# Optimization experiments

Hardware: AMD Instinct MI355X
Metric: run time of the kernel (lower is better)

Reference implementation:

```python
import jax, jax.numpy as jnp
import numpy as np
import math


def _silu(v):
    return v * jax.nn.sigmoid(v)


def setup_inputs() -> dict:
    key = jax.random.key(0)
    ks = jax.random.split(key, 8)
    b, l = 4, 2048
    dim, hidden, d_state, dt_rank = 1024, 2048, 16, 64
    s = 0.02
    x = jax.random.normal(ks[0], (b, l, dim), dtype=jnp.float32)
    W_in = jax.random.normal(ks[1], (2 * hidden, dim), dtype=jnp.float32) * s
    conv_w = jax.random.normal(ks[2], (hidden, 1, 3), dtype=jnp.float32) * s  # depthwise, k=3
    conv_b = jnp.zeros((hidden,), dtype=jnp.float32)
    W_xproj = jax.random.normal(ks[3], (dt_rank + 2 * d_state, hidden), dtype=jnp.float32) * s
    W_dt = jax.random.uniform(ks[4], (hidden, dt_rank), minval=-1.0 / dt_rank, maxval=1.0 / dt_rank, dtype=jnp.float32)
    dt_init = jnp.exp(jax.random.uniform(ks[5], (hidden,), dtype=jnp.float32) * (math.log(0.1) - math.log(0.001)) + math.log(0.001))
    b_dt = -1.0 / dt_init  # matches dt_proj.bias init in source
    A_log = -jnp.arange(1, d_state + 1, dtype=jnp.float32)
    D = jnp.ones((hidden,), dtype=jnp.float32)
    W_out = jax.random.normal(ks[6], (dim, hidden), dtype=jnp.float32) * s
    return {"x": x, "W_in": W_in, "conv_w": conv_w, "conv_b": conv_b,
            "W_xproj": W_xproj, "W_dt": W_dt, "b_dt": b_dt,
            "A_log": A_log, "D": D, "W_out": W_out}


def reference(x, W_in, conv_w, conv_b, W_xproj, W_dt, b_dt, A_log, D, W_out):
    b, l, dim = x.shape
    hidden = W_dt.shape[0]
    dt_rank = W_dt.shape[1]
    d_state = A_log.shape[0]

    # in_proj and chunk into (x, z)
    xz = jnp.einsum('bld,ed->ble', x, W_in)  # (b, l, 2*hidden)
    u, z = jnp.split(xz, 2, axis=-1)

    # depthwise conv1d, kernel 3, symmetric padding 1 (non-causal, as in source)
    uc = jax.lax.conv_general_dilated(
        jnp.moveaxis(u, 1, 2), conv_w, window_strides=(1,), padding=[(1, 1)],
        dimension_numbers=('NCH', 'OIH', 'NCH'), feature_group_count=hidden)
    uc = jnp.moveaxis(uc + conv_b[None, :, None], 1, 2)  # (b, l, hidden)
    uc = _silu(uc)

    # x_proj -> (dt, B, C)
    x_dbl = jnp.einsum('blh,eh->ble', uc, W_xproj)
    dtp = x_dbl[..., :dt_rank]
    Bm = x_dbl[..., dt_rank:dt_rank + d_state]   # (b, l, n)
    Cm = x_dbl[..., dt_rank + d_state:]          # (b, l, n)
    dt = jax.nn.softplus(jnp.einsum('blr,hr->blh', dtp, W_dt) + b_dt)  # (b, l, hidden)

    A = -jnp.exp(A_log)  # (n,)

    # selective scan: h_{k} = exp(dt_k * A) * h_{k-1} + B_k (outer) u_k ; y_k = C_k . h_k
    def step(h, inp):
        u_t, dt_t, B_t, C_t = inp  # (b,h), (b,h), (b,n), (b,n)
        dA = jnp.exp(dt_t[:, None, :] * A[None, :, None])      # (b, n, h)
        h = dA * h + B_t[:, :, None] * u_t[:, None, :]         # (b, n, h)
        y_t = jnp.einsum('bn,bnh->bh', C_t, h)
        return h, y_t

    xs = (jnp.moveaxis(uc, 0, 1), jnp.moveaxis(dt, 0, 1),
          jnp.moveaxis(Bm, 0, 1), jnp.moveaxis(Cm, 0, 1))
    h0 = jnp.zeros((b, d_state, hidden), dtype=uc.dtype)
    _, ys = jax.lax.scan(step, h0, xs)
    y = jnp.moveaxis(ys, 0, 1) + D * uc  # skip term D*u

    y = y * _silu(z)
    out = jnp.einsum('blh,dh->bld', y, W_out)
    return x + out
```

## Files before the change

### kernel.cpp

```cpp
#include <hip/hip_runtime.h>
#include <cmath>

typedef unsigned short u16;
typedef __bf16 bf16x8 __attribute__((ext_vector_type(8)));
typedef float f32x4 __attribute__((ext_vector_type(4)));
typedef unsigned short u16x8 __attribute__((ext_vector_type(8)));

#define NB_B   4
#define NB_L   2048
#define NB_DIM 1024
#define NB_H   2048
#define NB_NS  16
#define NB_DTR 64
#define NB_TOK (NB_B * NB_L)
#define NCHUNK 64
#define CLEN   32

__device__ __forceinline__ u16 f2b(float f) {
  union { float f; unsigned u; } v; v.f = f;
  unsigned r = v.u + 0x7fffu + ((v.u >> 16) & 1u);
  return (u16)(r >> 16);
}
__device__ __forceinline__ float b2f(u16 h) {
  union { unsigned u; float f; } v; v.u = ((unsigned)h) << 16;
  return v.f;
}
__device__ __forceinline__ float exp_small(float w) {
  return __builtin_fmaf(w, __builtin_fmaf(w, 0.5f, 1.0f), 1.0f);
}

#define CVT_N0 2097152
#define CVT_N1 (CVT_N0 + 1048576)
#define CVT_N2 (CVT_N1 + 32768)
#define CVT_N3 (CVT_N2 + 524288)
__global__ void cvt_all_k(const float* __restrict__ x, const float* __restrict__ W_in,
                          const float* __restrict__ W_dt, const float* __restrict__ W_out,
                          u16* __restrict__ xb, u16* __restrict__ winb,
                          u16* __restrict__ wdtb, u16* __restrict__ woutb) {
  int i = blockIdx.x * 256 + threadIdx.x;
  const float* src; u16* dst; int off;
  if (i < CVT_N0)      { src = x;     dst = xb;    off = i; }
  else if (i < CVT_N1) { src = W_in;  dst = winb;  off = i - CVT_N0; }
  else if (i < CVT_N2) { src = W_dt;  dst = wdtb;  off = i - CVT_N1; }
  else                 { src = W_out; dst = woutb; off = i - CVT_N2; }
  float4 v = reinterpret_cast<const float4*>(src)[off];
  ushort4 o;
  o.x = f2b(v.x); o.y = f2b(v.y); o.z = f2b(v.z); o.w = f2b(v.w);
  reinterpret_cast<ushort4*>(dst)[off] = o;
}

__global__ void cvt_pad_xproj_k(const float* __restrict__ in, u16* __restrict__ out) {
  int i = blockIdx.x * 256 + threadIdx.x;
  int r = i >> 11, c = i & 2047;
  out[i] = (r < 96) ? f2b(in[r * 2048 + c]) : (u16)0;
}

__global__ void extract_dtp_k(const float* __restrict__ xdbl, u16* __restrict__ out) {
  int i = blockIdx.x * 256 + threadIdx.x;
  int r = i >> 6, c = i & 63;
  out[i] = f2b(xdbl[r * 128 + c]);
}

#define EPI_BF16    0
#define EPI_F32     1
#define EPI_SP_BF16 2
#define EPI_RES_F32 3

__device__ __forceinline__ void stage16(const u16* g, u16* l) {
  __builtin_amdgcn_global_load_lds(
      (const __attribute__((address_space(1))) unsigned int*)g,
      (__attribute__((address_space(3))) unsigned int*)l, 16, 0, 0);
}

template <int EPI, int BM>
__global__ __launch_bounds__(512, 1)
void gemm8p_k(const u16* __restrict__ A, const u16* __restrict__ Bm,
              int K, int ldc,
              u16* __restrict__ outB, float* __restrict__ outF,
              const float* __restrict__ bias, const float* __restrict__ resid,
              int gx) {
  constexpr int BN = 256;
  constexpr int MR = BM / 32;
  constexpr int MH = MR / 2;
  constexpr int HA = BM / 2;
  constexpr int LA = BM / 128;
  constexpr int L  = 2 * LA + 4;
  constexpr int BUFE = (BM + BN) * 64;
  __shared__ u16 smem[2 * BUFE];

  const int tid  = threadIdx.x;
  const int lane = tid & 63;
  const int wave = tid >> 6;
  const int wr = wave >> 2, wc = wave & 3;
  const int fr = lane & 15, fq = lane >> 4;

  const int nwg = gridDim.x;
  const int cpx = nwg >> 3;
  const int bid = blockIdx.x;
  const int id2 = (bid & 7) * cpx + (bid >> 3);
  const int row0 = (id2 % gx) * BM;
  const int col0 = (id2 / gx) * BN;

  f32x4 acc[MR][4] = {};
  bf16x8 bB[4][2], bA0[MH][2], bA1[MH][2];

  auto STAGE_B = [&](int kt) {
    const int k0 = kt * 64;
    u16* base = smem + (kt & 1) * BUFE + BM * 64;
#pragma unroll
    for (int h = 0; h < 2; ++h)
#pragma unroll
      for (int l = 0; l < 2; ++l) {
        int c = l * 512 + tid;
        int rih = c >> 3, p = c & 7;
        stage16(Bm + (size_t)(col0 + h * 128 + rih) * K + k0 + ((p ^ (rih & 7)) * 8),
                base + (h * 128 + rih) * 64 + p * 8);
      }
  };
  auto STAGE_A = [&](int kt) {
    const int k0 = kt * 64;
    u16* base = smem + (kt & 1) * BUFE;
#pragma unroll
    for (int h = 0; h < 2; ++h)
#pragma unroll
      for (int l = 0; l < LA; ++l) {
        int c = l * 512 + tid;
        int rih = c >> 3, p = c & 7;
        stage16(A + (size_t)(row0 + h * HA + rih) * K + k0 + ((p ^ (rih & 7)) * 8),
                base + (h * HA + rih) * 64 + p * 8);
      }
  };
  auto LD_A = [&](int m, int kk, int bi) {
    int rt = wr * HA + m * 16 + fr;
    int p = (kk * 4 + fq) ^ (rt & 7);
    return *reinterpret_cast<const bf16x8*>(smem + bi * BUFE + rt * 64 + p * 8);
  };
  auto LD_B = [&](int n, int kk, int bi) {
    int rt = wc * 64 + n * 16 + fr;
    int p = (kk * 4 + fq) ^ (rt & 7);
    return *reinterpret_cast<const bf16x8*>(smem + bi * BUFE + BM * 64 + rt * 64 + p * 8);
  };

  const int nk = K >> 6;
  STAGE_B(0); STAGE_A(0);
  if (nk > 1) { STAGE_B(1); STAGE_A(1); }
  if (nk > 1) asm volatile("s_waitcnt vmcnt(%0)" :: "i"(L) : "memory");
  else        asm volatile("s_waitcnt vmcnt(0)" ::: "memory");
  __builtin_amdgcn_s_barrier();
  __builtin_amdgcn_sched_barrier(0);
#pragma unroll
  for (int n = 0; n < 4; ++n) { bB[n][0] = LD_B(n, 0, 0); bB[n][1] = LD_B(n, 1, 0); }
#pragma unroll
  for (int m = 0; m < MH; ++m) { bA0[m][0] = LD_A(m, 0, 0); bA0[m][1] = LD_A(m, 1, 0); }
  asm volatile("s_waitcnt lgkmcnt(0)" ::: "memory");
  __builtin_amdgcn_s_barrier();
  __builtin_amdgcn_sched_barrier(0);

  for (int kt = 0; kt < nk; ++kt) {
    const int bi = kt & 1;
    if (kt + 2 < nk) STAGE_B(kt + 2);
    __builtin_amdgcn_s_setprio(1);
#pragma unroll
    for (int m = 0; m < MH; ++m)
#pragma unroll
      for (int n = 0; n < 2; ++n)
#pragma unroll
        for (int kk = 0; kk < 2; ++kk)
          acc[m][n] = __builtin_amdgcn_mfma_f32_16x16x32_bf16(bA0[m][kk], bB[n][kk], acc[m][n], 0, 0, 0);
    __builtin_amdgcn_s_setprio(0);
    __builtin_amdgcn_sched_barrier(0);
#pragma unroll
    for (int m = 0; m < MH; ++m) { bA1[m][0] = LD_A(MH + m, 0, bi); bA1[m][1] = LD_A(MH + m, 1, bi); }
    __builtin_amdgcn_s_setprio(1);
#pragma unroll
    for (int m = 0; m < MH; ++m)
#pragma unroll
      for (int n = 2; n < 4; ++n)
#pragma unroll
        for (int kk = 0; kk < 2; ++kk)
          acc[m][n] = __builtin_amdgcn_mfma_f32_16x16x32_bf16(bA0[m][kk], bB[n][kk], acc[m][n], 0, 0, 0);
    __builtin_amdgcn_s_setprio(0);
    asm volatile("s_waitcnt lgkmcnt(0)" ::: "memory");
    __builtin_amdgcn_s_barrier();
    __builtin_amdgcn_sched_barrier(0);
    if (kt + 2 < nk) STAGE_A(kt + 2);
    __builtin_amdgcn_s_setprio(1);
#pragma unroll
    for (int m = 0; m < MH; ++m)
#pragma unroll
      for (int n = 0; n < 2; ++n)
#pragma unroll
        for (int kk = 0; kk < 2; ++kk)
          acc[MH + m][n] = __builtin_amdgcn_mfma_f32_16x16x32_bf16(bA1[m][kk], bB[n][kk], acc[MH + m][n], 0, 0, 0);
    __builtin_amdgcn_s_setprio(0);
    __builtin_amdgcn_sched_barrier(0);
    if (kt + 1 < nk) {
      if (kt + 2 < nk) asm volatile("s_waitcnt vmcnt(%0)" :: "i"(L) : "memory");
      else             asm volatile("s_waitcnt vmcnt(0)" ::: "memory");
      __builtin_amdgcn_s_barrier();
      __builtin_amdgcn_sched_barrier(0);
#pragma unroll
      for (int n = 0; n < 2; ++n) { bB[n][0] = LD_B(n, 0, bi ^ 1); bB[n][1] = LD_B(n, 1, bi ^ 1); }
#pragma unroll
      for (int m = 0; m < MH; ++m) { bA0[m][0] = LD_A(m, 0, bi ^ 1); bA0[m][1] = LD_A(m, 1, bi ^ 1); }
    }
    __builtin_amdgcn_s_setprio(1);
#pragma unroll
    for (int m = 0; m < MH; ++m)
#pragma unroll
      for (int n = 2; n < 4; ++n)
#pragma unroll
        for (int kk = 0; kk < 2; ++kk)
          acc[MH + m][n] = __builtin_amdgcn_mfma_f32_16x16x32_bf16(bA1[m][kk], bB[n][kk], acc[MH + m][n], 0, 0, 0);
    __builtin_amdgcn_s_setprio(0);
    if (kt + 1 < nk) {
#pragma unroll
      for (int n = 2; n < 4; ++n) { bB[n][0] = LD_B(n, 0, bi ^ 1); bB[n][1] = LD_B(n, 1, bi ^ 1); }
    }
    asm volatile("s_waitcnt lgkmcnt(0)" ::: "memory");
    __builtin_amdgcn_s_barrier();
    __builtin_amdgcn_sched_barrier(0);
  }

  if constexpr (EPI == EPI_BF16 || EPI == EPI_SP_BF16) {
    float* wv = reinterpret_cast<float*>(smem) + wave * 1024;
#pragma unroll
    for (int m = 0; m < MR; ++m) {
#pragma unroll
      for (int n = 0; n < 4; ++n) {
        const int c = col0 + wc * 64 + n * 16 + fr;
        float bv = (EPI == EPI_SP_BF16) ? bias[c] : 0.f;
#pragma unroll
        for (int j = 0; j < 4; ++j) {
          float v = acc[m][n][j];
          if (EPI == EPI_SP_BF16) {
            float xx = v + bv;
            float t = __expf(xx);
            float sp = (xx > -5.f) ? log1pf(t) : t;
            v = (xx > 20.f) ? xx : sp;
          }
          wv[(fq * 4 + j) * 64 + n * 16 + fr] = v;
        }
      }
#pragma unroll
      for (int p = 0; p < 2; ++p) {
        const int rf = p * 8 + (lane >> 3);
        const int c0 = (lane & 7) * 8;
        const float* rp = wv + rf * 64 + c0;
        u16x8 o;
#pragma unroll
        for (int k = 0; k < 8; ++k) o[k] = f2b(rp[k]);
        const int grow = row0 + wr * HA + m * 16 + rf;
        const int gcol = col0 + wc * 64 + c0;
        *reinterpret_cast<u16x8*>(&outB[(size_t)grow * ldc + gcol]) = o;
      }
    }
  } else {
#pragma unroll
    for (int m = 0; m < MR; ++m) {
      const int r = row0 + wr * HA + m * 16 + fq * 4;
#pragma unroll
      for (int n = 0; n < 4; ++n) {
        const int c = col0 + wc * 64 + n * 16 + fr;
#pragma unroll
        for (int j = 0; j < 4; ++j) {
          size_t o = (size_t)(r + j) * ldc + c;
          if (EPI == EPI_F32) outF[o] = acc[m][n][j];
          else                outF[o] = acc[m][n][j] + resid[o];
        }
      }
    }
  }
}

template <int EPI, int BM, int BN>
__global__ __launch_bounds__(256)
void gemm_bt_k(const u16* __restrict__ A, const u16* __restrict__ Bm,
               int K, int ldc,
               u16* __restrict__ outB, float* __restrict__ outF,
               const float* __restrict__ bias, const float* __restrict__ resid) {
  constexpr int MR = BM / 32, NR = BN / 32;
  __shared__ u16 smem[(BM + BN) * 32];
  u16* As = smem;
  u16* Bs = smem + BM * 32;
  const int tid  = threadIdx.x;
  const int lane = tid & 63;
  const int wave = tid >> 6;
  const int wr = wave >> 1, wc = wave & 1;
  const int row0 = blockIdx.x * BM;
  const int col0 = blockIdx.y * BN;
  f32x4 acc[MR][NR] = {};

  const int r_ld = tid >> 2;
  const int kb   = (((tid & 3) ^ ((tid >> 3) & 3)) * 8);
  const size_t a_base = (size_t)(row0 + r_ld) * K + kb;
  const size_t b_base = (size_t)(col0 + r_ld) * K + kb;
  u16* lA = As + tid * 8;
  u16* lB = Bs + tid * 8;

  const int fr = lane & 15;
  const int fq = lane >> 4;
  const int fkx = ((fq ^ ((fr >> 1) & 3)) * 8);

  const int nk = K >> 5;
  for (int kt = 0; kt < nk; ++kt) {
    const int k0 = kt * 32;
    __syncthreads();
#pragma unroll
    for (int hh = 0; hh < BM / 64; ++hh)
      stage16(A + a_base + (size_t)(hh * 64) * K + k0, lA + hh * 64 * 32);
#pragma unroll
    for (int hh = 0; hh < BN / 64; ++hh)
      stage16(Bm + b_base + (size_t)(hh * 64) * K + k0, lB + hh * 64 * 32);
    __syncthreads();
    bf16x8 af[MR], bfr[NR];
#pragma unroll
    for (int m = 0; m < MR; ++m)
      af[m] = *reinterpret_cast<const bf16x8*>(&As[(wr * (BM / 2) + m * 16 + fr) * 32 + fkx]);
#pragma unroll
    for (int n = 0; n < NR; ++n)
      bfr[n] = *reinterpret_cast<const bf16x8*>(&Bs[(wc * (BN / 2) + n * 16 + fr) * 32 + fkx]);
#pragma unroll
    for (int m = 0; m < MR; ++m)
#pragma unroll
      for (int n = 0; n < NR; ++n)
        acc[m][n] = __builtin_amdgcn_mfma_f32_16x16x32_bf16(af[m], bfr[n], acc[m][n], 0, 0, 0);
  }

#pragma unroll
  for (int m = 0; m < MR; ++m) {
    const int r = row0 + wr * (BM / 2) + m * 16 + fq * 4;
#pragma unroll
    for (int n = 0; n < NR; ++n) {
      const int c = col0 + wc * (BN / 2) + n * 16 + fr;
#pragma unroll
      for (int j = 0; j < 4; ++j) {
        float v = acc[m][n][j];
        size_t o = (size_t)(r + j) * ldc + c;
        if (EPI == EPI_F32) outF[o] = v;
        else if (EPI == EPI_RES_F32) outF[o] = v + resid[o];
      }
    }
  }
}

__global__ void dwconv_silu_k(const u16* __restrict__ xz, const float* __restrict__ cw,
                              const float* __restrict__ cb, u16* __restrict__ uc) {
  int i = blockIdx.x * 256 + threadIdx.x;
  int hb = i & (NB_H / 8 - 1);
  int t = i >> 8;
  int l = t & (NB_L - 1);
  int h0 = hb * 8;
  const u16* base = xz + (size_t)t * 4096 + h0;
  u16x8 vm = *reinterpret_cast<const u16x8*>(base);
  u16x8 vq = {}, vp = {};
  if (l > 0)          vq = *reinterpret_cast<const u16x8*>(base - 4096);
  if (l < NB_L - 1)   vp = *reinterpret_cast<const u16x8*>(base + 4096);
  u16x8 o;
#pragma unroll
  for (int j = 0; j < 8; ++j) {
    int h = h0 + j;
    float acc = cb[h];
    acc = __builtin_fmaf(b2f(vq[j]), cw[h * 3 + 0], acc);
    acc = __builtin_fmaf(b2f(vm[j]), cw[h * 3 + 1], acc);
    acc = __builtin_fmaf(b2f(vp[j]), cw[h * 3 + 2], acc);
    float s = acc / (1.f + __expf(-acc));
    o[j] = f2b(s);
  }
  *reinterpret_cast<u16x8*>(uc + (size_t)t * NB_H + h0) = o;
}

__global__ __launch_bounds__(256)
void scan_passA_k(const u16* __restrict__ dt, const u16* __restrict__ uc,
                  const float* __restrict__ xdbl, const float* __restrict__ A_log,
                  float* __restrict__ Pout, float* __restrict__ Sout) {
  __shared__ float bc[CLEN][32];
  const int tid = threadIdx.x;
  int idx = blockIdx.x * 256 + tid;
  int h = idx & (NB_H - 1);
  int ck = (idx >> 11) & (NCHUNK - 1);
  int b = idx >> 17;
  const int t0 = b * NB_L + ck * CLEN;
  {
    int r = tid >> 3, q = tid & 7;
    *reinterpret_cast<float4*>(&bc[r][q * 4]) =
        *reinterpret_cast<const float4*>(xdbl + (size_t)(t0 + r) * 128 + 64 + q * 4);
  }
  float An[NB_NS];
#pragma unroll
  for (int n = 0; n < NB_NS; ++n) An[n] = -__expf(A_log[n]);
  float P[NB_NS], S[NB_NS];
#pragma unroll
  for (int n = 0; n < NB_NS; ++n) { P[n] = 1.f; S[n] = 0.f; }
  __syncthreads();
  const u16* up = uc + (size_t)t0 * NB_H + h;
  const u16* dp = dt + (size_t)t0 * NB_H + h;
  float uA = b2f(up[0]),       dA = b2f(dp[0]);
  float uB = b2f(up[NB_H]),    dB = b2f(dp[NB_H]);
  for (int tt = 0; tt < CLEN; ++tt) {
    float uC = 0.f, dC = 0.f;
    if (tt + 2 < CLEN) { uC = b2f(up[2 * NB_H]); dC = b2f(dp[2 * NB_H]); }
    up += NB_H; dp += NB_H;
    float4 B0 = *reinterpret_cast<const float4*>(&bc[tt][0]);
    float4 B1 = *reinterpret_cast<const float4*>(&bc[tt][4]);
    float4 B2 = *reinterpret_cast<const float4*>(&bc[tt][8]);
    float4 B3 = *reinterpret_cast<const float4*>(&bc[tt][12]);
    const float Bf[NB_NS] = {B0.x, B0.y, B0.z, B0.w, B1.x, B1.y, B1.z, B1.w,
                             B2.x, B2.y, B2.z, B2.w, B3.x, B3.y, B3.z, B3.w};
#pragma unroll
    for (int n = 0; n < NB_NS; ++n) {
      float e = exp_small(dA * An[n]);
      P[n] *= e;
      S[n] = __builtin_fmaf(e, S[n], Bf[n] * uA);
    }
    uA = uB; dA = dB; uB = uC; dB = dC;
  }
#pragma unroll
  for (int n = 0; n < NB_NS; ++n) {
    size_t o = ((((size_t)b * NCHUNK + ck) * NB_NS + n) * NB_H + h);
    Pout[o] = P[n]; Sout[o] = S[n];
  }
}

__global__ void scan_passB_k(float* __restrict__ P, const float* __restrict__ S) {
  int idx = blockIdx.x * 256 + threadIdx.x;
  int h = idx & (NB_H - 1);
  int n = (idx >> 11) & (NB_NS - 1);
  int b = idx >> 15;
  const size_t stride = (size_t)NB_NS * NB_H;
  size_t o = ((size_t)b * NCHUNK * NB_NS + n) * NB_H + h;
  float hs = 0.f;
  float p0 = P[o], s0 = S[o];
  for (int ck = 0; ck < NCHUNK; ++ck) {
    float p1 = 0.f, s1 = 0.f;
    if (ck + 1 < NCHUNK) { p1 = P[o + stride]; s1 = S[o + stride]; }
    P[o] = hs;
    hs = __builtin_fmaf(p0, hs, s0);
    o += stride; p0 = p1; s0 = s1;
  }
}

__global__ __launch_bounds__(256)
void scan_passC_k(const u16* __restrict__ dt, const u16* __restrict__ uc,
                  const float* __restrict__ xdbl, const u16* __restrict__ xz,
                  const float* __restrict__ A_log, const float* __restrict__ Dp,
                  const float* __restrict__ Hst, u16* __restrict__ ybf) {
  __shared__ float bc[CLEN][32];
  const int tid = threadIdx.x;
  int idx = blockIdx.x * 256 + tid;
  int h = idx & (NB_H - 1);
  int ck = (idx >> 11) & (NCHUNK - 1);
  int b = idx >> 17;
  const int t0 = b * NB_L + ck * CLEN;
  {
    int r = tid >> 3, q = tid & 7;
    *reinterpret_cast<float4*>(&bc[r][q * 4]) =
        *reinterpret_cast<const float4*>(xdbl + (size_t)(t0 + r) * 128 + 64 + q * 4);
  }
  float An[NB_NS];
#pragma unroll
  for (int n = 0; n < NB_NS; ++n) An[n] = -__expf(A_log[n]);
  float s[NB_NS];
#pragma unroll
  for (int n = 0; n < NB_NS; ++n)
    s[n] = Hst[((((size_t)b * NCHUNK + ck) * NB_NS + n) * NB_H + h)];
  const float Dh = Dp[h];
  __syncthreads();
  const u16* up = uc + (size_t)t0 * NB_H + h;
  const u16* dp = dt + (size_t)t0 * NB_H + h;
  const u16* zp = xz + (size_t)t0 * 4096 + NB_H + h;
  u16* yp = ybf + (size_t)t0 * NB_H + h;
  float uA = b2f(up[0]),    dA = b2f(dp[0]),    zA = b2f(zp[0]);
  float uB = b2f(up[NB_H]), dB = b2f(dp[NB_H]), zB = b2f(zp[4096]);
  for (int tt = 0; tt < CLEN; ++tt) {
    float uC = 0.f, dC = 0.f, zC = 0.f;
    if (tt + 2 < CLEN) {
      uC = b2f(up[2 * NB_H]); dC = b2f(dp[2 * NB_H]); zC = b2f(zp[2 * 4096]);
    }
    up += NB_H; dp += NB_H; zp += 4096;
    float4 B0 = *reinterpret_cast<const float4*>(&bc[tt][0]);
    float4 B1 = *reinterpret_cast<const float4*>(&bc[tt][4]);
    float4 B2 = *reinterpret_cast<const float4*>(&bc[tt][8]);
    float4 B3 = *reinterpret_cast<const float4*>(&bc[tt][12]);
    float4 C0 = *reinterpret_cast<const float4*>(&bc[tt][16]);
    float4 C1 = *reinterpret_cast<const float4*>(&bc[tt][20]);
    float4 C2 = *reinterpret_cast<const float4*>(&bc[tt][24]);
    float4 C3 = *reinterpret_cast<const float4*>(&bc[tt][28]);
    const float Bf[NB_NS] = {B0.x, B0.y, B0.z, B0.w, B1.x, B1.y, B1.z, B1.w,
                             B2.x, B2.y, B2.z, B2.w, B3.x, B3.y, B3.z, B3.w};
    const float Cf[NB_NS] = {C0.x, C0.y, C0.z, C0.w, C1.x, C1.y, C1.z, C1.w,
                             C2.x, C2.y, C2.z, C2.w, C3.x, C3.y, C3.z, C3.w};
    float y = 0.f;
#pragma unroll
    for (int n = 0; n < NB_NS; ++n) {
      float e = exp_small(dA * An[n]);
      s[n] = __builtin_fmaf(e, s[n], Bf[n] * uA);
      y = __builtin_fmaf(Cf[n], s[n], y);
    }
    float v = __builtin_fmaf(Dh, uA, y);
    float g = zA / (1.f + __expf(-zA));
    *yp = f2b(v * g);
    yp += NB_H;
    uA = uB; dA = dB; zA = zB; uB = uC; dB = dC; zB = zC;
  }
}

extern "C" void kernel_launch(void* const* d_in, const int* in_sizes, int n_in,
                              void* d_out, int out_size, void* d_ws, size_t ws_size,
                              hipStream_t stream) {
  const float* x      = (const float*)d_in[0];
  const float* W_in   = (const float*)d_in[1];
  const float* conv_w = (const float*)d_in[2];
  const float* conv_b = (const float*)d_in[3];
  const float* W_xprj = (const float*)d_in[4];
  const float* W_dt   = (const float*)d_in[5];
  const float* b_dt   = (const float*)d_in[6];
  const float* A_log  = (const float*)d_in[7];
  const float* Dp     = (const float*)d_in[8];
  const float* W_out  = (const float*)d_in[9];
  float* out = (float*)d_out;

  char* ws = (char*)d_ws;
  size_t off = 0;
  auto alloc = [&](size_t bytes) {
    void* p = ws + off;
    off += (bytes + 255) & ~(size_t)255;
    return p;
  };
  u16*   xz_b   = (u16*)alloc((size_t)NB_TOK * 4096 * 2);
  u16*   x_b    = (u16*)alloc((size_t)NB_TOK * NB_DIM * 2);
  u16*   win_b  = (u16*)alloc((size_t)4096 * NB_DIM * 2);
  u16*   wxp_b  = (u16*)alloc((size_t)128 * NB_H * 2);
  u16*   wdt_b  = (u16*)alloc((size_t)NB_H * NB_DTR * 2);
  u16*   wout_b = (u16*)alloc((size_t)NB_DIM * NB_H * 2);
  u16*   uc_b   = (u16*)alloc((size_t)NB_TOK * NB_H * 2);
  float* xdbl   = (float*)alloc((size_t)NB_TOK * 128 * 4);
  u16*   dtp_b  = (u16*)alloc((size_t)NB_TOK * NB_DTR * 2);
  u16*   dt_b   = (u16*)alloc((size_t)NB_TOK * NB_H * 2);
  float* scP    = (float*)alloc((size_t)NB_B * NCHUNK * NB_NS * NB_H * 4);
  float* scS    = (float*)alloc((size_t)NB_B * NCHUNK * NB_NS * NB_H * 4);
  u16*   y_b    = (u16*)scS;
  (void)ws_size; (void)in_sizes; (void)n_in; (void)out_size;

  cvt_all_k<<<CVT_N3 / 256, 256, 0, stream>>>(x, W_in, W_dt, W_out, x_b, win_b, wdt_b, wout_b);
  cvt_pad_xproj_k<<<1024, 256, 0, stream>>>(W_xprj, wxp_b);

  gemm8p_k<EPI_BF16, 256><<<512, 512, 0, stream>>>(
      x_b, win_b, NB_DIM, 4096, xz_b, nullptr, nullptr, nullptr, 32);

  dwconv_silu_k<<<(NB_TOK * NB_H / 8) / 256, 256, 0, stream>>>(xz_b, conv_w, conv_b, uc_b);

  gemm_bt_k<EPI_F32, 64, 64><<<dim3(128, 2), 256, 0, stream>>>(
      uc_b, wxp_b, NB_H, 128, nullptr, xdbl, nullptr, nullptr);

  extract_dtp_k<<<(NB_TOK * NB_DTR) / 256, 256, 0, stream>>>(xdbl, dtp_b);

  gemm8p_k<EPI_SP_BF16, 256><<<256, 512, 0, stream>>>(
      dtp_b, wdt_b, NB_DTR, NB_H, dt_b, nullptr, b_dt, nullptr, 32);

  scan_passA_k<<<(NB_B * NCHUNK * NB_H) / 256, 256, 0, stream>>>(dt_b, uc_b, xdbl, A_log, scP, scS);
  scan_passB_k<<<(NB_B * NB_NS * NB_H) / 256, 256, 0, stream>>>(scP, scS);
  scan_passC_k<<<(NB_B * NCHUNK * NB_H) / 256, 256, 0, stream>>>(dt_b, uc_b, xdbl, xz_b, A_log, Dp, scP, y_b);

  gemm8p_k<EPI_RES_F32, 128><<<256, 512, 0, stream>>>(
      y_b, wout_b, NB_H, NB_DIM, nullptr, out, nullptr, x, 64);
}
```

Before: 349.0 us.

## Store scan chunk states in bf16, remap GEMM tiles per XCD, pack epilogue as bf16

The chunk-state buffers exchanged between the three scan passes are stored as bf16 instead of fp32, with the decay product kept as 1-P to preserve precision near one. This halves the traffic between the passes. Each GEMM workgroup now maps to a tile region chosen per XCD (cr/cc/ncx parameters) so tiles on the same die share A and B panels in L2. The bf16 epilogue also converts before staging through padded LDS, which halves LDS traffic. The scan-state rounding to bf16 risks accuracy loss over 64 chunks.

```diff
diff --git a/kernel.cpp b/kernel.cpp
--- a/kernel.cpp
+++ b/kernel.cpp
@@ -78,14 +78,13 @@
               int K, int ldc,
               u16* __restrict__ outB, float* __restrict__ outF,
               const float* __restrict__ bias, const float* __restrict__ resid,
-              int gx) {
-  constexpr int BN = 256;
+              int cr, int cc, int ncx) {
   constexpr int MR = BM / 32;
   constexpr int MH = MR / 2;
   constexpr int HA = BM / 2;
   constexpr int LA = BM / 128;
   constexpr int L  = 2 * LA + 4;
-  constexpr int BUFE = (BM + BN) * 64;
+  constexpr int BUFE = (BM + 256) * 64;
   __shared__ u16 smem[2 * BUFE];
 
   const int tid  = threadIdx.x;
@@ -94,12 +93,10 @@
   const int wr = wave >> 2, wc = wave & 3;
   const int fr = lane & 15, fq = lane >> 4;
 
-  const int nwg = gridDim.x;
-  const int cpx = nwg >> 3;
   const int bid = blockIdx.x;
-  const int id2 = (bid & 7) * cpx + (bid >> 3);
-  const int row0 = (id2 % gx) * BM;
-  const int col0 = (id2 / gx) * BN;
+  const int e = bid & 7, w = bid >> 3;
+  const int row0 = ((e / ncx) * cr + (w % cr)) * BM;
+  const int col0 = ((e % ncx) * cc + (w / cr)) * 256;
 
   f32x4 acc[MR][4] = {};
   bf16x8 bB[4][2], bA0[MH][2], bA1[MH][2];
@@ -223,7 +220,7 @@
   }
 
   if constexpr (EPI == EPI_BF16 || EPI == EPI_SP_BF16) {
-    float* wv = reinterpret_cast<float*>(smem) + wave * 1024;
+    u16* wv = smem + wave * 1152;
 #pragma unroll
     for (int m = 0; m < MR; ++m) {
 #pragma unroll
@@ -239,20 +236,17 @@
             float sp = (xx > -5.f) ? log1pf(t) : t;
             v = (xx > 20.f) ? xx : sp;
           }
-          wv[(fq * 4 + j) * 64 + n * 16 + fr] = v;
+          wv[(fq * 4 + j) * 72 + n * 16 + fr] = f2b(v);
         }
       }
 #pragma unroll
       for (int p = 0; p < 2; ++p) {
         const int rf = p * 8 + (lane >> 3);
         const int c0 = (lane & 7) * 8;
-        const float* rp = wv + rf * 64 + c0;
-        u16x8 o;
-#pragma unroll
-        for (int k = 0; k < 8; ++k) o[k] = f2b(rp[k]);
+        u16x8 ov = *reinterpret_cast<const u16x8*>(wv + rf * 72 + c0);
         const int grow = row0 + wr * HA + m * 16 + rf;
         const int gcol = col0 + wc * 64 + c0;
-        *reinterpret_cast<u16x8*>(&outB[(size_t)grow * ldc + gcol]) = o;
+        *reinterpret_cast<u16x8*>(&outB[(size_t)grow * ldc + gcol]) = ov;
       }
     }
   } else {
@@ -373,7 +367,7 @@
 __global__ __launch_bounds__(256)
 void scan_passA_k(const u16* __restrict__ dt, const u16* __restrict__ uc,
                   const float* __restrict__ xdbl, const float* __restrict__ A_log,
-                  float* __restrict__ Pout, float* __restrict__ Sout) {
+                  u16* __restrict__ dPout, u16* __restrict__ Sout) {
   __shared__ float bc[CLEN][32];
   const int tid = threadIdx.x;
   int idx = blockIdx.x * 256 + tid;
@@ -418,11 +412,12 @@
 #pragma unroll
   for (int n = 0; n < NB_NS; ++n) {
     size_t o = ((((size_t)b * NCHUNK + ck) * NB_NS + n) * NB_H + h);
-    Pout[o] = P[n]; Sout[o] = S[n];
-  }
-}
-
-__global__ void scan_passB_k(float* __restrict__ P, const float* __restrict__ S) {
+    dPout[o] = f2b(1.0f - P[n]);
+    Sout[o]  = f2b(S[n]);
+  }
+}
+
+__global__ void scan_passB_k(u16* __restrict__ dP, const u16* __restrict__ S) {
   int idx = blockIdx.x * 256 + threadIdx.x;
   int h = idx & (NB_H - 1);
   int n = (idx >> 11) & (NB_NS - 1);
@@ -430,11 +425,11 @@
   const size_t stride = (size_t)NB_NS * NB_H;
   size_t o = ((size_t)b * NCHUNK * NB_NS + n) * NB_H + h;
   float hs = 0.f;
-  float p0 = P[o], s0 = S[o];
+  float p0 = 1.f - b2f(dP[o]), s0 = b2f(S[o]);
   for (int ck = 0; ck < NCHUNK; ++ck) {
-    float p1 = 0.f, s1 = 0.f;
-    if (ck + 1 < NCHUNK) { p1 = P[o + stride]; s1 = S[o + stride]; }
-    P[o] = hs;
+    float p1 = 1.f, s1 = 0.f;
+    if (ck + 1 < NCHUNK) { p1 = 1.f - b2f(dP[o + stride]); s1 = b2f(S[o + stride]); }
+    dP[o] = f2b(hs);
     hs = __builtin_fmaf(p0, hs, s0);
     o += stride; p0 = p1; s0 = s1;
   }
@@ -444,7 +439,7 @@
 void scan_passC_k(const u16* __restrict__ dt, const u16* __restrict__ uc,
                   const float* __restrict__ xdbl, const u16* __restrict__ xz,
                   const float* __restrict__ A_log, const float* __restrict__ Dp,
-                  const float* __restrict__ Hst, u16* __restrict__ ybf) {
+                  const u16* __restrict__ Hst, u16* __restrict__ ybf) {
   __shared__ float bc[CLEN][32];
   const int tid = threadIdx.x;
   int idx = blockIdx.x * 256 + tid;
@@ -463,7 +458,7 @@
   float s[NB_NS];
 #pragma unroll
   for (int n = 0; n < NB_NS; ++n)
-    s[n] = Hst[((((size_t)b * NCHUNK + ck) * NB_NS + n) * NB_H + h)];
+    s[n] = b2f(Hst[((((size_t)b * NCHUNK + ck) * NB_NS + n) * NB_H + h)]);
   const float Dh = Dp[h];
   __syncthreads();
   const u16* up = uc + (size_t)t0 * NB_H + h;
@@ -537,16 +532,16 @@
   float* xdbl   = (float*)alloc((size_t)NB_TOK * 128 * 4);
   u16*   dtp_b  = (u16*)alloc((size_t)NB_TOK * NB_DTR * 2);
   u16*   dt_b   = (u16*)alloc((size_t)NB_TOK * NB_H * 2);
-  float* scP    = (float*)alloc((size_t)NB_B * NCHUNK * NB_NS * NB_H * 4);
-  float* scS    = (float*)alloc((size_t)NB_B * NCHUNK * NB_NS * NB_H * 4);
-  u16*   y_b    = (u16*)scS;
+  u16*   scdP   = (u16*)alloc((size_t)NB_B * NCHUNK * NB_NS * NB_H * 2);
+  u16*   scS    = (u16*)alloc((size_t)NB_B * NCHUNK * NB_NS * NB_H * 2);
+  u16*   y_b    = (u16*)alloc((size_t)NB_TOK * NB_H * 2);
   (void)ws_size; (void)in_sizes; (void)n_in; (void)out_size;
 
   cvt_all_k<<<CVT_N3 / 256, 256, 0, stream>>>(x, W_in, W_dt, W_out, x_b, win_b, wdt_b, wout_b);
   cvt_pad_xproj_k<<<1024, 256, 0, stream>>>(W_xprj, wxp_b);
 
   gemm8p_k<EPI_BF16, 256><<<512, 512, 0, stream>>>(
-      x_b, win_b, NB_DIM, 4096, xz_b, nullptr, nullptr, nullptr, 32);
+      x_b, win_b, NB_DIM, 4096, xz_b, nullptr, nullptr, nullptr, 8, 8, 2);
 
   dwconv_silu_k<<<(NB_TOK * NB_H / 8) / 256, 256, 0, stream>>>(xz_b, conv_w, conv_b, uc_b);
 
@@ -556,12 +551,12 @@
   extract_dtp_k<<<(NB_TOK * NB_DTR) / 256, 256, 0, stream>>>(xdbl, dtp_b);
 
   gemm8p_k<EPI_SP_BF16, 256><<<256, 512, 0, stream>>>(
-      dtp_b, wdt_b, NB_DTR, NB_H, dt_b, nullptr, b_dt, nullptr, 32);
-
-  scan_passA_k<<<(NB_B * NCHUNK * NB_H) / 256, 256, 0, stream>>>(dt_b, uc_b, xdbl, A_log, scP, scS);
-  scan_passB_k<<<(NB_B * NB_NS * NB_H) / 256, 256, 0, stream>>>(scP, scS);
-  scan_passC_k<<<(NB_B * NCHUNK * NB_H) / 256, 256, 0, stream>>>(dt_b, uc_b, xdbl, xz_b, A_log, Dp, scP, y_b);
+      dtp_b, wdt_b, NB_DTR, NB_H, dt_b, nullptr, b_dt, nullptr, 4, 8, 1);
+
+  scan_passA_k<<<(NB_B * NCHUNK * NB_H) / 256, 256, 0, stream>>>(dt_b, uc_b, xdbl, A_log, scdP, scS);
+  scan_passB_k<<<(NB_B * NB_NS * NB_H) / 256, 256, 0, stream>>>(scdP, scS);
+  scan_passC_k<<<(NB_B * NCHUNK * NB_H) / 256, 256, 0, stream>>>(dt_b, uc_b, xdbl, xz_b, A_log, Dp, scdP, y_b);
 
   gemm8p_k<EPI_RES_F32, 128><<<256, 512, 0, stream>>>(
-      y_b, wout_b, NB_H, NB_DIM, nullptr, out, nullptr, x, 64);
-}
+      y_b, wout_b, NB_H, NB_DIM, nullptr, out, nullptr, x, 8, 4, 1);
+}
```

New measurement: 340.2 us. -2.5%, faster.
